# Performance work log

Measured on AMD Instinct MI355X. Metric: run time of the kernel, lower is better.

## Reference

```python
import jax, jax.numpy as jnp
import numpy as np

EPS = 1e-5


def _silu(x):
    return x * jax.nn.sigmoid(x)


def _bn(x, g, b, m, v):
    # x: [N, C, H, W], eval-mode batchnorm with running stats
    scale = (g / jnp.sqrt(v + EPS))[None, :, None, None]
    shift = (b - m * g / jnp.sqrt(v + EPS))[None, :, None, None]
    return x * scale + shift


def setup_inputs() -> dict:
    key = jax.random.key(0)
    ks = jax.random.split(key, 24)
    B, C, H, W = 4, 256, 128, 128
    Q, E, S = 256, 192, 4  # query_dim, evidence_channels, n_stems
    std = 0.02
    inp = {
        "memory": jax.random.normal(ks[0], (B, C, H, W), jnp.float32),
        "active_mask": jax.random.bernoulli(ks[1], 0.7, (B, S)),
        "stem_query": jax.random.normal(ks[2], (S, Q), jnp.float32) * std,
        "memory_proj_w": jax.random.normal(ks[3], (Q, C), jnp.float32) * std,
        "in_proj_w": jax.random.normal(ks[4], (3 * Q, Q), jnp.float32) * std,
        "in_proj_b": jnp.zeros((3 * Q,), jnp.float32),
        "out_proj_w": jax.random.normal(ks[5], (Q, Q), jnp.float32) * std,
        "out_proj_b": jnp.zeros((Q,), jnp.float32),
        "ev_w": jax.random.normal(ks[6], (E, C), jnp.float32) * std,
        "bn1_g": jax.random.uniform(ks[7], (E,), jnp.float32, 0.5, 1.5),
        "bn1_b": jax.random.normal(ks[8], (E,), jnp.float32) * 0.1,
        "bn1_m": jax.random.normal(ks[9], (E,), jnp.float32) * 0.1,
        "bn1_v": jax.random.uniform(ks[10], (E,), jnp.float32, 0.5, 1.5),
        "gate_w": jax.random.normal(ks[11], (E, Q), jnp.float32) * std,
        "gate_b": jnp.zeros((E,), jnp.float32),
        "film_w": jax.random.normal(ks[12], (2 * E, Q), jnp.float32) * std,
        "film_b": jnp.zeros((2 * E,), jnp.float32),
        "out_w": jax.random.normal(ks[13], (E, E, 3, 3), jnp.float32) * std,
        "bn2_g": jax.random.uniform(ks[14], (E,), jnp.float32, 0.5, 1.5),
        "bn2_b": jax.random.normal(ks[15], (E,), jnp.float32) * 0.1,
        "bn2_m": jax.random.normal(ks[16], (E,), jnp.float32) * 0.1,
        "bn2_v": jax.random.uniform(ks[17], (E,), jnp.float32, 0.5, 1.5),
    }
    return inp


def reference(memory, active_mask, stem_query, memory_proj_w, in_proj_w, in_proj_b,
              out_proj_w, out_proj_b, ev_w, bn1_g, bn1_b, bn1_m, bn1_v,
              gate_w, gate_b, film_w, film_b, out_w, bn2_g, bn2_b, bn2_m, bn2_v):
    B, C, H, W = memory.shape
    St, Qd = stem_query.shape
    E = ev_w.shape[0]
    nh = 4
    dh = Qd // nh

    # memory_proj (1x1 conv) -> tokens [B, HW, Q]
    mt = jnp.einsum('bchw,qc->bqhw', memory, memory_proj_w)  # memory_tokens
    tokens = mt.reshape(B, Qd, H * W).transpose(0, 2, 1)

    # Multihead cross-attention: one query per stem over all samples.
    Wq, Wk, Wv = jnp.split(in_proj_w, 3, axis=0)
    bq, bk, bv = jnp.split(in_proj_b, 3, axis=0)
    q = (stem_query @ Wq.T + bq).reshape(St, nh, dh)            # [St, nh, dh]
    k = (tokens @ Wk.T + bk).reshape(B, H * W, nh, dh)          # [B, S, nh, dh]
    v = (tokens @ Wv.T + bv).reshape(B, H * W, nh, dh)
    scores = jnp.einsum('tnd,bsnd->tbns', q, k) / jnp.sqrt(jnp.asarray(dh, q.dtype))
    attw = jax.nn.softmax(scores, axis=-1)
    attended = jnp.einsum('tbns,bsnd->tbnd', attw, v).reshape(St, B, Qd)
    state = attended @ out_proj_w.T + out_proj_b               # [St, B, Q]

    # Stem-independent evidence and gate (math identical per gathered sample).
    evidence = _silu(_bn(jnp.einsum('bchw,ec->behw', memory, ev_w),
                         bn1_g, bn1_b, bn1_m, bn1_v))          # [B, E, H, W]
    gate = jax.nn.sigmoid(jnp.einsum('bqhw,eq->behw', mt, gate_w)
                          + gate_b[None, :, None, None])       # [B, E, H, W]

    # FiLM per stem
    gb = state @ film_w.T + film_b                             # [St, B, 2E]
    gamma, beta = gb[..., :E], gb[..., E:]
    x = (evidence[None] * gate[None] * (1.0 + gamma[..., None, None])
         + beta[..., None, None])                              # [St, B, E, H, W]

    # out: 3x3 conv -> BN -> SiLU, applied over flattened (stem, batch)
    xf = x.reshape(St * B, E, H, W)
    y = jax.lax.conv_general_dilated(xf, out_w, (1, 1), 'SAME',
                                     dimension_numbers=('NCHW', 'OIHW', 'NCHW'))
    u = _silu(_bn(y, bn2_g, bn2_b, bn2_m, bn2_v)).reshape(St, B, E, H, W)

    # scatter semantics: zero-out inactive (stem, sample) slots
    m = active_mask.T.astype(u.dtype)[:, :, None, None, None]  # [St, B, 1, 1, 1]
    return u * m
```

## Files before the change

kernel.cpp:

```cpp
#include <hip/hip_runtime.h>
#include <hip/hip_bf16.h>

#define EPSV 1e-5f

typedef __attribute__((ext_vector_type(8))) short short8;
typedef __attribute__((ext_vector_type(4))) float f32x4;

__device__ __forceinline__ float bf2f(short u) {
    union { float f; unsigned v; } x; x.v = ((unsigned)(unsigned short)u) << 16; return x.f;
}
__device__ __forceinline__ short f2bf(float f) {
    union { float f; unsigned v; } x; x.f = f;
    unsigned r = x.v + 0x7FFFu + ((x.v >> 16) & 1u);
    return (short)(r >> 16);
}

#define GLDS(gp, lp) __builtin_amdgcn_global_load_lds( \
    (const __attribute__((address_space(1))) unsigned int*)(gp), \
    (__attribute__((address_space(3))) unsigned int*)(lp), 16, 0, 0)

__global__ __launch_bounds__(256) void make_wbig(
    const float* evw, const float* bn1g, const float* bn1b, const float* bn1m, const float* bn1v,
    const float* gatew, const float* gateb, const float* ipw, const float* ipb, const float* mpw,
    short* Wbig, float* biasBig)
{
    __shared__ float w1[256];
    int r = blockIdx.x, c = threadIdx.x;
    if (r < 384 && (r & 1) == 0) {
        int e = r >> 1;
        float s1 = bn1g[e] * rsqrtf(bn1v[e] + EPSV);
        Wbig[r * 256 + c] = f2bf(evw[e * 256 + c] * s1);
        if (c == 0) biasBig[r] = bn1b[e] - bn1m[e] * s1;
    } else {
        const float* src; float bias;
        if (r < 384)      { int e = r >> 1; src = gatew + e * 256; bias = gateb[e]; }
        else if (r < 640) { src = ipw + (256 + (r - 384)) * 256;  bias = ipb[256 + (r - 384)]; }
        else              { src = ipw + (512 + (r - 640)) * 256;  bias = ipb[512 + (r - 640)]; }
        w1[c] = src[c];
        __syncthreads();
        float a = 0.f;
        #pragma unroll 8
        for (int q = 0; q < 256; ++q) a += w1[q] * mpw[q * 256 + c];
        Wbig[r * 256 + c] = f2bf(a);
        if (c == 0) biasBig[r] = bias;
    }
}

__global__ __launch_bounds__(256) void make_wfold(
    const float* outw, const float* g2, const float* b2, const float* m2, const float* v2,
    short* Wfold, float* t2, float* zp)
{
    int f = blockIdx.x;
    if (f >= 192) {
        int blk = f - 192;
        *(f32x4*)(zp + (blk * 256 + threadIdx.x) * 4) = f32x4{0.f, 0.f, 0.f, 0.f};
        return;
    }
    float s2 = g2[f] * rsqrtf(v2[f] + EPSV);
    for (int idx = threadIdx.x; idx < 1728; idx += 256) {
        int e = idx / 9, tap = idx % 9;
        Wfold[(tap * 192 + f) * 192 + e] = f2bf(outw[(f * 192 + e) * 9 + tap] * s2);
    }
    if (threadIdx.x == 0) t2[f] = b2[f] - m2[f] * s2;
}

__global__ __launch_bounds__(256) void make_q(const float* sq, const float* ipw, const float* ipb,
                                              const void* raw, float* qout, float* maskf)
{
    int t = blockIdx.x;
    if (t == 4) {
        if (threadIdx.x != 0) return;
        const unsigned* w = (const unsigned*)raw;
        const unsigned char* by = (const unsigned char*)raw;
        bool stride4 = true;
        for (int i = 0; i < 4; ++i) {
            unsigned x = w[i];
            if (!(x == 0u || x == 1u || x == 0x3F800000u)) stride4 = false;
        }
        float vals[16];
        if (stride4) { for (int i = 0; i < 16; ++i) vals[i] = (w[i] != 0u) ? 1.f : 0.f; }
        else         { for (int i = 0; i < 16; ++i) vals[i] = (by[i] != 0) ? 1.f : 0.f; }
        for (int tt = 0; tt < 4; ++tt)
            for (int b = 0; b < 4; ++b)
                maskf[tt * 4 + b] = vals[b * 4 + tt];
        return;
    }
    int i = threadIdx.x;
    float a = ipb[i];
    for (int cc = 0; cc < 256; ++cc) a += sq[t * 256 + cc] * ipw[i * 256 + cc];
    qout[t * 256 + i] = a * 0.125f;
}

__global__ __launch_bounds__(256) void transpose_mem(const float* mem, short* memT)
{
    __shared__ float tile[64][65];
    int hw0 = blockIdx.x * 64, c0 = blockIdx.y * 64, b = blockIdx.z;
    const float* src = mem + (size_t)(b * 256 + c0) * 16384 + hw0;
    #pragma unroll
    for (int j = 0; j < 16; ++j) {
        int idx = threadIdx.x + j * 256;
        int r = idx >> 6, wcol = idx & 63;
        tile[r][wcol] = src[(size_t)r * 16384 + wcol];
    }
    __syncthreads();
    short* dst = memT + (size_t)(b * 16384 + hw0) * 256 + c0;
    #pragma unroll
    for (int j = 0; j < 16; ++j) {
        int idx = threadIdx.x + j * 256;
        int r = idx >> 6, wcol = idx & 63;
        dst[(size_t)r * 256 + wcol] = f2bf(tile[wcol][r]);
    }
}

__global__ __launch_bounds__(256) void big_gemm(const short* memT, const short* Wbig,
                                                const float* biasBig, short* P2, short* KV)
{
    __shared__ __align__(16) short As[128 * 64];
    __shared__ __align__(16) short Bs[128 * 64];
    int tid = threadIdx.x, lane = tid & 63, wid = tid >> 6;
    int hw0 = blockIdx.x * 128, n0 = blockIdx.y * 128, b = blockIdx.z;
    int wm = wid & 1, wn = wid >> 1;
    f32x4 acc[4][4];
    #pragma unroll
    for (int i = 0; i < 4; ++i)
        #pragma unroll
        for (int j = 0; j < 4; ++j)
            #pragma unroll
            for (int r = 0; r < 4; ++r) acc[i][j][r] = 0.f;

    int r8 = lane >> 3, c8 = lane & 7;
    int cs = c8 ^ r8;
    const short* Abase = memT + (size_t)(b * 16384 + hw0) * 256 + cs * 8;
    const short* Bbase = Wbig + (size_t)n0 * 256 + cs * 8;

    for (int kk = 0; kk < 256; kk += 64) {
        #pragma unroll
        for (int s = 0; s < 4; ++s) {
            int seg = wid * 4 + s;
            int row = seg * 8 + r8;
            GLDS(Abase + (size_t)row * 256 + kk, As + seg * 512);
            GLDS(Bbase + (size_t)row * 256 + kk, Bs + seg * 512);
        }
        __syncthreads();
        #pragma unroll
        for (int ks = 0; ks < 2; ++ks) {
            short8 af[4], bfr[4];
            #pragma unroll
            for (int mt = 0; mt < 4; ++mt) {
                int row = wm * 64 + mt * 16 + (lane & 15);
                af[mt] = *(const short8*)((char*)As + ((row * 128 + ks * 64 + (lane >> 4) * 16) ^ ((row & 7) << 4)));
            }
            #pragma unroll
            for (int nt = 0; nt < 4; ++nt) {
                int col = wn * 64 + nt * 16 + (lane & 15);
                bfr[nt] = *(const short8*)((char*)Bs + ((col * 128 + ks * 64 + (lane >> 4) * 16) ^ ((col & 7) << 4)));
            }
            #pragma unroll
            for (int mt = 0; mt < 4; ++mt)
                #pragma unroll
                for (int nt = 0; nt < 4; ++nt)
                    acc[mt][nt] = __builtin_amdgcn_mfma_f32_16x16x32_bf16(af[mt], bfr[nt], acc[mt][nt], 0, 0, 0);
        }
        __syncthreads();
    }
    if (n0 < 384) {
        #pragma unroll
        for (int nt = 0; nt < 4; ++nt) {
            int col = n0 + wn * 64 + nt * 16 + (lane & 15);
            float bias = biasBig[col];
            int e = col >> 1;
            short* pplane = P2 + ((size_t)(b * 24 + (e >> 3)) * 16384) * 8 + (e & 7);
            #pragma unroll
            for (int mt = 0; mt < 4; ++mt) {
                int hwbase = hw0 + wm * 64 + mt * 16 + (lane >> 4) * 4;
                #pragma unroll
                for (int r = 0; r < 4; ++r) {
                    float v = acc[mt][nt][r] + bias;
                    float p = __shfl_xor(v, 1);
                    if ((lane & 1) == 0) {
                        float se = 1.f / (1.f + __expf(-v));
                        float sg = 1.f / (1.f + __expf(-p));
                        pplane[(size_t)(hwbase + r) * 8] = f2bf(v * se * sg);
                    }
                }
            }
        }
    } else {
        #pragma unroll
        for (int nt = 0; nt < 4; ++nt) {
            int col = n0 + wn * 64 + nt * 16 + (lane & 15);
            float bias = biasBig[col];
            int kcol = col - 384;
            #pragma unroll
            for (int mt = 0; mt < 4; ++mt) {
                int hwbase = hw0 + wm * 64 + mt * 16 + (lane >> 4) * 4;
                #pragma unroll
                for (int r = 0; r < 4; ++r)
                    KV[(size_t)(b * 16384 + hwbase + r) * 512 + kcol] = f2bf(acc[mt][nt][r] + bias);
            }
        }
    }
}

__global__ __launch_bounds__(256) void attn_a(const short* KV, const float* qs,
                                              float* Opart, float* Lpart)
{
    __shared__ float qlds[256];
    __shared__ float Esm[4 * 512];
    __shared__ float wl[4][4];
    __shared__ short vlds[128 * 72];
    int tid = threadIdx.x, lane = tid & 63, wid = tid >> 6;
    int chunk = blockIdx.x, n = blockIdx.y, b = blockIdx.z;
    int s0 = chunk * 512;
    qlds[tid] = qs[(tid >> 6) * 256 + n * 64 + (tid & 63)];
    __syncthreads();
    float lp[4] = {0.f, 0.f, 0.f, 0.f};
    #pragma unroll
    for (int half = 0; half < 2; ++half) {
        int s = s0 + half * 256 + tid;
        const short* kb = KV + (size_t)(b * 16384 + s) * 512 + n * 64;
        float sc[4] = {0.f, 0.f, 0.f, 0.f};
        #pragma unroll
        for (int i = 0; i < 8; ++i) {
            short8 k8 = *(const short8*)(kb + i * 8);
            #pragma unroll
            for (int j = 0; j < 8; ++j) {
                float kf = bf2f(k8[j]);
                #pragma unroll
                for (int t = 0; t < 4; ++t) sc[t] += kf * qlds[t * 64 + i * 8 + j];
            }
        }
        #pragma unroll
        for (int t = 0; t < 4; ++t) {
            float e = __expf(sc[t]);
            Esm[t * 512 + half * 256 + tid] = e;
            lp[t] += e;
        }
    }
    #pragma unroll
    for (int t = 0; t < 4; ++t) {
        float v = lp[t];
        for (int off = 32; off; off >>= 1) v += __shfl_down(v, off);
        if (lane == 0) wl[wid][t] = v;
    }
    __syncthreads();
    if (tid < 4)
        Lpart[((b * 4 + n) * 32 + chunk) * 4 + tid] = wl[0][tid] + wl[1][tid] + wl[2][tid] + wl[3][tid];

    float o = 0.f;
    int tt = tid >> 6, d = tid & 63;
    for (int sub = 0; sub < 4; ++sub) {
        __syncthreads();
        #pragma unroll
        for (int j = 0; j < 4; ++j) {
            int idx = tid + j * 256;
            int r = idx >> 3, c16 = idx & 7;
            const short* vb = KV + (size_t)(b * 16384 + s0 + sub * 128 + r) * 512 + 256 + n * 64 + c16 * 8;
            *(short8*)((char*)vlds + r * 144 + c16 * 16) = *(const short8*)vb;
        }
        __syncthreads();
        #pragma unroll 8
        for (int r = 0; r < 128; ++r)
            o += Esm[tt * 512 + sub * 128 + r] * bf2f(vlds[r * 72 + d]);
    }
    Opart[(size_t)((b * 4 + n) * 32 + chunk) * 256 + tid] = o;
}

__global__ __launch_bounds__(256) void attn_b(const float* Opart, const float* Lpart, float* attended)
{
    int bn = blockIdx.x;
    int tid = threadIdx.x, t = tid >> 6, d = tid & 63;
    float o = 0.f, l = 0.f;
    for (int c = 0; c < 32; ++c) o += Opart[(size_t)(bn * 32 + c) * 256 + tid];
    for (int c = 0; c < 32; ++c) l += Lpart[(bn * 32 + c) * 4 + t];
    int b = bn >> 2, n = bn & 3;
    attended[(t * 4 + b) * 256 + n * 64 + d] = o / l;
}

__global__ __launch_bounds__(256) void film_kernel(const float* attended, const float* opw, const float* opb,
                                                   const float* fw, const float* fb,
                                                   float* Afilm, float* Bfilm)
{
    __shared__ float att[256], st[256];
    int tb = blockIdx.x, tid = threadIdx.x;
    att[tid] = attended[tb * 256 + tid];
    __syncthreads();
    float a = opb[tid];
    for (int j = 0; j < 256; ++j) a += att[j] * opw[tid * 256 + j];
    st[tid] = a;
    __syncthreads();
    float g1 = fb[tid];
    for (int j = 0; j < 256; ++j) g1 += st[j] * fw[tid * 256 + j];
    if (tid < 192) Afilm[tb * 192 + tid] = 1.f + g1;
    else           Bfilm[tb * 192 + (tid - 192)] = g1;
    if (tid < 128) {
        int jj = 256 + tid;
        float g2 = fb[jj];
        for (int j = 0; j < 256; ++j) g2 += st[j] * fw[jj * 256 + j];
        Bfilm[tb * 192 + (jj - 192)] = g2;
    }
}

__global__ __launch_bounds__(256) void make_w2(const short* Wfold, const float* Afilm, short* W2L)
{
    __shared__ float A[192];
    int tb = blockIdx.x, tap = blockIdx.y;
    if (threadIdx.x < 192) A[threadIdx.x] = Afilm[tb * 192 + threadIdx.x];
    __syncthreads();
    for (int u = threadIdx.x; u < 4608; u += 256) {
        int ec = u / 768, rem = u % 768, f16 = rem >> 6, l = rem & 63;
        int f = f16 * 16 + (l & 15), e0 = ec * 32 + (l >> 4) * 8;
        short8 wv = *(const short8*)(Wfold + (tap * 192 + f) * 192 + e0);
        short8 o;
        #pragma unroll
        for (int j = 0; j < 8; ++j) o[j] = f2bf(bf2f(wv[j]) * A[e0 + j]);
        *(short8*)(W2L + ((((size_t)(tb * 6 + ec) * 9 + tap) * 12 + f16) * 64 + l) * 8) = o;
    }
}

__global__ __launch_bounds__(256) void make_btab(const short* Wfold, const float* Bfilm, float* Btab)
{
    __shared__ short Wt[192 * 192];
    __shared__ float Bv[16][192];
    int tap = blockIdx.x, tid = threadIdx.x;
    for (int u = tid; u < 4608; u += 256)
        *(short8*)(Wt + u * 8) = *(const short8*)(Wfold + (size_t)tap * 36864 + u * 8);
    for (int u = tid; u < 3072; u += 256) Bv[u / 192][u % 192] = Bfilm[u];
    __syncthreads();
    for (int o = tid; o < 3072; o += 256) {
        int tb = o / 192, f = o % 192;
        const short* wr = Wt + f * 192;
        float a = 0.f;
        #pragma unroll 8
        for (int e = 0; e < 192; ++e) a += bf2f(wr[e]) * Bv[tb][e];
        Btab[((size_t)tb * 9 + tap) * 192 + f] = a;
    }
}

__global__ __launch_bounds__(256, 2) void conv2_kernel(const short* P2, const short* W2L, const float* t2,
                                                       const float* Btab, const float* maskf,
                                                       const short* zp, float* out)
{
    __shared__ __align__(16) short XB[2][12480];
    __shared__ float biasC[192], cLs[192], cRs[192];
    int tid = threadIdx.x, lane = tid & 63, wid = tid >> 6;
    int i = blockIdx.x + blockIdx.y * 128;
    int n = (i & 7) * 256 + (i >> 3);
    int h = n & 127, tb = n >> 7;
    int b = tb & 3;
    float m = maskf[tb];
    float* obase = out + (size_t)tb * 192 * 16384 + h * 128;
    if (m == 0.f) {
        #pragma unroll
        for (int it = 0; it < 96; ++it) {
            int idx = tid + it * 256;
            int f = idx >> 7, w = idx & 127;
            obase[(size_t)f * 16384 + w] = 0.f;
        }
        return;
    }
    if (tid < 192) {
        const float* T = Btab + (size_t)tb * 1728 + tid;
        float s0 = T[0], s1 = T[192], s2v = T[384], s3 = T[576], s4 = T[768];
        float s5 = T[960], s6 = T[1152], s7 = T[1344], s8 = T[1536];
        float bc = s0 + s1 + s2v + s3 + s4 + s5 + s6 + s7 + s8;
        float l = s0 + s3 + s6, r = s2v + s5 + s8;
        if (h == 0)   { bc -= s0 + s1 + s2v; l -= s0; r -= s2v; }
        if (h == 127) { bc -= s6 + s7 + s8; l -= s6; r -= s8; }
        biasC[tid] = bc; cLs[tid] = l; cRs[tid] = r;
    }
    f32x4 acc[3][8];
    #pragma unroll
    for (int a = 0; a < 3; ++a)
        #pragma unroll
        for (int c = 0; c < 8; ++c)
            #pragma unroll
            for (int r = 0; r < 4; ++r) acc[a][c][r] = 0.f;

    short* buf0 = &XB[0][0];
    short* buf1 = &XB[1][0];

    auto STAGE = [&](short* buf, int ec) {
        #pragma unroll
        for (int s = 0; s < 3; ++s) {
            int seg = wid * 3 + s, row = seg >> 2, eu = seg & 3;
            int habs = h + row - 1;
            bool hok = (unsigned)habs < 128u;
            const short* plane = P2 + ((size_t)(b * 24 + ec * 4 + eu) * 16384) * 8;
            long hbase = (long)habs * 128 - 1;
            short* ldst = buf + seg * 1040;
            const short* a0 = (hok && lane > 0) ? plane + (hbase + lane) * 8       : zp + lane * 8;
            const short* a1 = hok               ? plane + (hbase + 64 + lane) * 8  : zp + 1024 + lane * 8;
            GLDS(a0, ldst);
            GLDS(a1, ldst + 512);
            if (lane < 2) {
                const short* a2 = (hok && lane < 1) ? plane + (hbase + 128 + lane) * 8 : zp + 2048 + lane * 8;
                GLDS(a2, ldst + 1024);
            }
        }
    };
    const short* wbase = W2L + (size_t)tb * 331776 + (wid * 3) * 512 + lane * 8;

    STAGE(buf0, 0);
    __syncthreads();
    #pragma unroll
    for (int t = 0; t < 6; ++t) {
        const short* cur = (t & 1) ? buf1 : buf0;
        short* nxt = (t & 1) ? buf0 : buf1;

        const short* wec = wbase + (size_t)t * 55296;
        short8 af[27];
        #pragma unroll
        for (int tap = 0; tap < 9; ++tap)
            #pragma unroll
            for (int ft = 0; ft < 3; ++ft)
                af[tap * 3 + ft] = *(const short8*)(wec + tap * 6144 + ft * 512);
        __builtin_amdgcn_sched_barrier(0);
        if (t < 5) STAGE(nxt, t + 1);

        __builtin_amdgcn_s_setprio(1);
        #pragma unroll
        for (int tap = 0; tap < 9; ++tap) {
            int dy = tap / 3, dx = tap % 3;
            const short* xrow = cur + ((dy * 4 + (lane >> 4)) * 130 + (lane & 15) + dx) * 8;
            #pragma unroll
            for (int wt = 0; wt < 8; ++wt) {
                short8 xb = *(const short8*)(xrow + wt * 128);
                #pragma unroll
                for (int ft = 0; ft < 3; ++ft)
                    acc[ft][wt] = __builtin_amdgcn_mfma_f32_16x16x32_bf16(af[tap * 3 + ft], xb, acc[ft][wt], 0, 0, 0);
            }
        }
        __builtin_amdgcn_s_setprio(0);
        if (t < 5) __syncthreads();
    }

    #pragma unroll
    for (int ft = 0; ft < 3; ++ft)
        #pragma unroll
        for (int r = 0; r < 4; ++r) {
            int f = wid * 48 + ft * 16 + (lane >> 4) * 4 + r;
            float bc = biasC[f] + t2[f];
            float lf = cLs[f], rg = cRs[f];
            #pragma unroll
            for (int wt = 0; wt < 8; ++wt) {
                int w = wt * 16 + (lane & 15);
                float val = acc[ft][wt][r] + bc;
                if (w == 0)   val -= lf;
                if (w == 127) val -= rg;
                obase[(size_t)f * 16384 + w] = val / (1.f + __expf(-val)) * m;
            }
        }
}

__global__ __launch_bounds__(256) void conv_kernel(const short* P2, const short* Wfold, const float* t2,
                                                   const float* Afilm, const float* Bfilm, const float* maskf,
                                                   float* out)
{
    __shared__ short Xs[3 * 130 * 32];
    __shared__ float Af[192], Bf[192];
    int tid = threadIdx.x, lane = tid & 63, wid = tid >> 6;
    int h = blockIdx.x, tb = blockIdx.y;
    int b = tb & 3;
    float* obase = out + (size_t)tb * 192 * 16384 + h * 128;
    float m = maskf[tb];
    if (m == 0.f) {
        #pragma unroll
        for (int i = 0; i < 96; ++i) {
            int idx = tid + i * 256;
            int f = idx >> 7, w = idx & 127;
            obase[(size_t)f * 16384 + w] = 0.f;
        }
        return;
    }
    if (tid < 192) { Af[tid] = Afilm[tb * 192 + tid]; Bf[tid] = Bfilm[tb * 192 + tid]; }
    f32x4 acc[3][8];
    #pragma unroll
    for (int i = 0; i < 3; ++i)
        #pragma unroll
        for (int j = 0; j < 8; ++j)
            #pragma unroll
            for (int r = 0; r < 4; ++r) acc[i][j][r] = 0.f;
    __syncthreads();

    for (int ec = 0; ec < 6; ++ec) {
        #pragma unroll
        for (int it = 0; it < 7; ++it) {
            int u = tid + it * 256;
            if (u < 1560) {
                int pos = u >> 2, half = u & 3;
                int row = (pos >= 260) ? 2 : (pos >= 130 ? 1 : 0);
                int col = pos - row * 130;
                int habs = h + row - 1;
                int w = col - 1;
                short8 x8 = {0, 0, 0, 0, 0, 0, 0, 0};
                if ((unsigned)habs < 128u && (unsigned)w < 128u) {
                    int e0 = ec * 32 + half * 8;
                    short8 pv = *(const short8*)(P2 + ((size_t)(b * 24 + (e0 >> 3)) * 16384 + habs * 128 + w) * 8);
                    #pragma unroll
                    for (int i = 0; i < 8; ++i)
                        x8[i] = f2bf(bf2f(pv[i]) * Af[e0 + i] + Bf[e0 + i]);
                }
                *(short8*)((char*)Xs + (((row * 130 + col) * 64 + half * 16) ^ ((col & 7) << 4))) = x8;
            }
        }
        __syncthreads();
        #pragma unroll
        for (int tap = 0; tap < 9; ++tap) {
            int dy = tap / 3, dx = tap % 3;
            short8 af[3];
            #pragma unroll
            for (int ft = 0; ft < 3; ++ft) {
                int f = wid * 48 + ft * 16 + (lane & 15);
                af[ft] = *(const short8*)(Wfold + (tap * 192 + f) * 192 + ec * 32 + (lane >> 4) * 8);
            }
            #pragma unroll
            for (int wt = 0; wt < 8; ++wt) {
                int cs = wt * 16 + (lane & 15) + dx;
                short8 bfr = *(const short8*)((char*)Xs + (((dy * 130 + cs) * 64 + (lane >> 4) * 16) ^ ((cs & 7) << 4)));
                #pragma unroll
                for (int ft = 0; ft < 3; ++ft)
                    acc[ft][wt] = __builtin_amdgcn_mfma_f32_16x16x32_bf16(af[ft], bfr, acc[ft][wt], 0, 0, 0);
            }
        }
        __syncthreads();
    }
    #pragma unroll
    for (int ft = 0; ft < 3; ++ft)
        #pragma unroll
        for (int wt = 0; wt < 8; ++wt) {
            int w = wt * 16 + (lane & 15);
            #pragma unroll
            for (int r = 0; r < 4; ++r) {
                int f = wid * 48 + ft * 16 + (lane >> 4) * 4 + r;
                float val = acc[ft][wt][r] + t2[f];
                obase[(size_t)f * 16384 + w] = val / (1.f + __expf(-val)) * m;
            }
        }
}

extern "C" void kernel_launch(void* const* d_in, const int* in_sizes, int n_in,
                              void* d_out, int out_size, void* d_ws, size_t ws_size,
                              hipStream_t stream)
{
    (void)in_sizes; (void)n_in; (void)out_size;
    const float* memory = (const float*)d_in[0];
    const void*  mask   = d_in[1];
    const float* sq     = (const float*)d_in[2];
    const float* mpw    = (const float*)d_in[3];
    const float* ipw    = (const float*)d_in[4];
    const float* ipb    = (const float*)d_in[5];
    const float* opw    = (const float*)d_in[6];
    const float* opb    = (const float*)d_in[7];
    const float* evw    = (const float*)d_in[8];
    const float* bn1g   = (const float*)d_in[9];
    const float* bn1b   = (const float*)d_in[10];
    const float* bn1m   = (const float*)d_in[11];
    const float* bn1v   = (const float*)d_in[12];
    const float* gatew  = (const float*)d_in[13];
    const float* gateb  = (const float*)d_in[14];
    const float* filmw  = (const float*)d_in[15];
    const float* filmb  = (const float*)d_in[16];
    const float* outw   = (const float*)d_in[17];
    const float* bn2g   = (const float*)d_in[18];
    const float* bn2b   = (const float*)d_in[19];
    const float* bn2m   = (const float*)d_in[20];
    const float* bn2v   = (const float*)d_in[21];

    char* ws = (char*)d_ws;
    short* P        = (short*)(ws + 65536);
    short* Wbig     = (short*)(ws + 25296896);
    float* biasBig  = (float*)(ws + 25755648);
    short* Wfold    = (short*)(ws + 25759232);
    float* t2       = (float*)(ws + 26422784);
    float* qs       = (float*)(ws + 26423552);
    float* attended = (float*)(ws + 26427648);
    float* Afilm    = (float*)(ws + 26431744);
    float* Bfilm    = (float*)(ws + 26444032);
    float* maskf    = (float*)(ws + 26456320);
    float* Lpart    = (float*)(ws + 26456576);
    short* W2       = (short*)(ws + 26464768);
    float* Btab     = (float*)(ws + 37081600);
    const size_t WS_NEED = 37204480;

    char* ob = (char*)d_out;
    short* KV     = (short*)(ob);
    short* memT   = (short*)(ob + 67108864);
    float* Opart  = (float*)(ob + 100663296);

    make_wbig<<<896, 256, 0, stream>>>(evw, bn1g, bn1b, bn1m, bn1v, gatew, gateb, ipw, ipb, mpw, Wbig, biasBig);
    make_wfold<<<208, 256, 0, stream>>>(outw, bn2g, bn2b, bn2m, bn2v, Wfold, t2, (float*)ws);
    make_q<<<5, 256, 0, stream>>>(sq, ipw, ipb, mask, qs, maskf);
    transpose_mem<<<dim3(256, 4, 4), 256, 0, stream>>>(memory, memT);
    big_gemm<<<dim3(128, 7, 4), 256, 0, stream>>>(memT, Wbig, biasBig, P, KV);
    attn_a<<<dim3(32, 4, 4), 256, 0, stream>>>(KV, qs, Opart, Lpart);
    attn_b<<<16, 256, 0, stream>>>(Opart, Lpart, attended);
    film_kernel<<<16, 256, 0, stream>>>(attended, opw, opb, filmw, filmb, Afilm, Bfilm);

    if (ws_size >= WS_NEED) {
        make_w2<<<dim3(16, 9), 256, 0, stream>>>(Wfold, Afilm, W2);
        make_btab<<<9, 256, 0, stream>>>(Wfold, Bfilm, Btab);
        conv2_kernel<<<dim3(128, 16), 256, 0, stream>>>(P, W2, t2, Btab, maskf, (const short*)ws, (float*)d_out);
    } else {
        conv_kernel<<<dim3(128, 16), 256, 0, stream>>>(P, Wfold, t2, Afilm, Bfilm, maskf, (float*)d_out);
    }
}
```

Measured before the change: 401.0 us.

## Read conv input directly from global memory instead of LDS double buffering

Removes the LDS double-buffered staging of the input halo rows (global_load_lds plus barriers) in the 3x3 conv kernel. Each lane now loads its input vectors straight from global memory, relying on cache for reuse across taps and waves. Weights are loaded per tap instead of all 27 fragments up front, which lowers register pressure. The cost is more global/L2 traffic and exposed load latency, since there is no explicit prefetch overlap with the MFMAs.

```diff
diff --git a/kernel.cpp b/kernel.cpp
--- a/kernel.cpp
+++ b/kernel.cpp
@@ -341,7 +341,6 @@
                                                        const float* Btab, const float* maskf,
                                                        const short* zp, float* out)
 {
-    __shared__ __align__(16) short XB[2][12480];
     __shared__ float biasC[192], cLs[192], cRs[192];
     int tid = threadIdx.x, lane = tid & 63, wid = tid >> 6;
     int i = blockIdx.x + blockIdx.y * 128;
@@ -369,6 +368,8 @@
         if (h == 127) { bc -= s6 + s7 + s8; l -= s6; r -= s8; }
         biasC[tid] = bc; cLs[tid] = l; cRs[tid] = r;
     }
+    __syncthreads();
+
     f32x4 acc[3][8];
     #pragma unroll
     for (int a = 0; a < 3; ++a)
@@ -377,62 +378,43 @@
             #pragma unroll
             for (int r = 0; r < 4; ++r) acc[a][c][r] = 0.f;
 
-    short* buf0 = &XB[0][0];
-    short* buf1 = &XB[1][0];
-
-    auto STAGE = [&](short* buf, int ec) {
-        #pragma unroll
-        for (int s = 0; s < 3; ++s) {
-            int seg = wid * 3 + s, row = seg >> 2, eu = seg & 3;
-            int habs = h + row - 1;
-            bool hok = (unsigned)habs < 128u;
-            const short* plane = P2 + ((size_t)(b * 24 + ec * 4 + eu) * 16384) * 8;
-            long hbase = (long)habs * 128 - 1;
-            short* ldst = buf + seg * 1040;
-            const short* a0 = (hok && lane > 0) ? plane + (hbase + lane) * 8       : zp + lane * 8;
-            const short* a1 = hok               ? plane + (hbase + 64 + lane) * 8  : zp + 1024 + lane * 8;
-            GLDS(a0, ldst);
-            GLDS(a1, ldst + 512);
-            if (lane < 2) {
-                const short* a2 = (hok && lane < 1) ? plane + (hbase + 128 + lane) * 8 : zp + 2048 + lane * 8;
-                GLDS(a2, ldst + 1024);
-            }
-        }
-    };
+    int cl = lane & 15, q = lane >> 4;
+    int hoff[3]; bool hok[3];
+    #pragma unroll
+    for (int dy = 0; dy < 3; ++dy) {
+        int habs = h + dy - 1;
+        hok[dy] = (unsigned)habs < 128u;
+        hoff[dy] = habs * 128;
+    }
+    const short* pbq = P2 + ((size_t)(b * 24 + q) * 16384) * 8;
     const short* wbase = W2L + (size_t)tb * 331776 + (wid * 3) * 512 + lane * 8;
 
-    STAGE(buf0, 0);
-    __syncthreads();
-    #pragma unroll
-    for (int t = 0; t < 6; ++t) {
-        const short* cur = (t & 1) ? buf1 : buf0;
-        short* nxt = (t & 1) ? buf0 : buf1;
-
-        const short* wec = wbase + (size_t)t * 55296;
-        short8 af[27];
-        #pragma unroll
-        for (int tap = 0; tap < 9; ++tap)
-            #pragma unroll
-            for (int ft = 0; ft < 3; ++ft)
-                af[tap * 3 + ft] = *(const short8*)(wec + tap * 6144 + ft * 512);
-        __builtin_amdgcn_sched_barrier(0);
-        if (t < 5) STAGE(nxt, t + 1);
-
+    for (int ec = 0; ec < 6; ++ec) {
+        const short* pe = pbq + (size_t)ec * 4 * 16384 * 8;
+        const short* wec = wbase + (size_t)ec * 55296;
         __builtin_amdgcn_s_setprio(1);
         #pragma unroll
         for (int tap = 0; tap < 9; ++tap) {
             int dy = tap / 3, dx = tap % 3;
-            const short* xrow = cur + ((dy * 4 + (lane >> 4)) * 130 + (lane & 15) + dx) * 8;
+            short8 af[3];
+            #pragma unroll
+            for (int ft = 0; ft < 3; ++ft)
+                af[ft] = *(const short8*)(wec + tap * 6144 + ft * 512);
+            int wb = cl + dx - 1;
+            const short* rowp = pe + (size_t)hoff[dy] * 8;
+            bool rowok = hok[dy];
             #pragma unroll
             for (int wt = 0; wt < 8; ++wt) {
-                short8 xb = *(const short8*)(xrow + wt * 128);
+                int wcol = wt * 16 + wb;
+                bool ok = rowok && ((unsigned)wcol < 128u);
+                const short* xa = ok ? rowp + (size_t)wcol * 8 : zp;
+                short8 xb = *(const short8*)xa;
                 #pragma unroll
                 for (int ft = 0; ft < 3; ++ft)
-                    acc[ft][wt] = __builtin_amdgcn_mfma_f32_16x16x32_bf16(af[tap * 3 + ft], xb, acc[ft][wt], 0, 0, 0);
+                    acc[ft][wt] = __builtin_amdgcn_mfma_f32_16x16x32_bf16(af[ft], xb, acc[ft][wt], 0, 0, 0);
             }
         }
         __builtin_amdgcn_s_setprio(0);
-        if (t < 5) __syncthreads();
     }
 
     #pragma unroll
```

Result: slower. 491.0 us (+22.4%).
